# Kernel optimization log

Measured on AMD Instinct MI355X. Metric: run time of the kernel, lower is better.

The kernel has to match this reference:

```python
import jax, jax.numpy as jnp
import numpy as np

B, T, ENC_C = 64, 512, 512   # batch, encoder frames, encoder channels
H = 512                      # hidden_channels
D = 80                       # out_channels (mel dim)
RF = 2                       # reduction_factor
PRE_IN = D * RF              # prenet input (= D*2, see go_frame)
PRE_INNER = 256
CONV_CH = 32                 # location conv channels
K = 31                       # location conv kernel size


def setup_inputs():
    key = jax.random.key(0)
    ks = jax.random.split(key, 16)
    s = 0.02
    f32 = jnp.float32
    p = {}
    p['enc_output'] = jax.random.normal(ks[0], (B, T, ENC_C), f32)
    # acoustic lengths in [T, 2T], multiples of RF -> len//RF in [T//2, T]
    p['data_len'] = (jax.random.randint(ks[1], (B,), T // 2, T + 1, jnp.int32) * RF).astype(jnp.int32)
    # Prenet: two 1x1 convs (== linears) + ReLU
    p['pn_w1'] = jax.random.normal(ks[2], (PRE_INNER, PRE_IN), f32) * s
    p['pn_b1'] = jnp.zeros((PRE_INNER,), f32)
    p['pn_w2'] = jax.random.normal(ks[3], (H, PRE_INNER), f32) * s
    p['pn_b2'] = jnp.zeros((H,), f32)
    # Location-sensitive attention
    p['att_enc_w'] = jax.random.normal(ks[4], (H, ENC_C), f32) * s
    p['att_enc_b'] = jnp.zeros((H,), f32)
    p['att_dec_w'] = jax.random.normal(ks[5], (H, H), f32) * s
    p['att_conv_w'] = jax.random.normal(ks[6], (CONV_CH, 1, K), f32) * s
    p['att_loc_w'] = jax.random.normal(ks[7], (H, CONV_CH), f32) * s
    p['att_v_w'] = jax.random.normal(ks[8], (H,), f32) * s
    p['att_v_b'] = jnp.zeros((), f32)
    # 2 GRU cells (torch GRUCell layout: gates [r|z|n])
    p['gru0_wih'] = jax.random.normal(ks[9], (3 * H, ENC_C + H), f32) * s
    p['gru0_whh'] = jax.random.normal(ks[10], (3 * H, H), f32) * s
    p['gru0_bih'] = jnp.zeros((3 * H,), f32)
    p['gru0_bhh'] = jnp.zeros((3 * H,), f32)
    p['gru1_wih'] = jax.random.normal(ks[11], (3 * H, H), f32) * s
    p['gru1_whh'] = jax.random.normal(ks[12], (3 * H, H), f32) * s
    p['gru1_bih'] = jnp.zeros((3 * H,), f32)
    p['gru1_bhh'] = jnp.zeros((3 * H,), f32)
    # out_layer: 1x1 Conv1d(2H -> D*RF) == linear
    p['out_w'] = jax.random.normal(ks[13], (D * RF, 2 * H), f32) * s
    p['out_b'] = jnp.zeros((D * RF,), f32)
    return p


def _gru(x, h, wih, whh, bih, bhh):
    gi = x @ wih.T + bih
    gh = h @ whh.T + bhh
    ir, iz, inn = jnp.split(gi, 3, axis=-1)
    hr, hz, hn = jnp.split(gh, 3, axis=-1)
    r = jax.nn.sigmoid(ir + hr)
    z = jax.nn.sigmoid(iz + hz)
    n = jnp.tanh(inn + r * hn)
    return (1.0 - z) * n + z * h


def _decode(enc_output, data_len, pn_w1, pn_b1, pn_w2, pn_b2,
            att_enc_w, att_enc_b, att_dec_w, att_conv_w, att_loc_w, att_v_w, att_v_b,
            gru0_wih, gru0_whh, gru0_bih, gru0_bhh,
            gru1_wih, gru1_whh, gru1_bih, gru1_bhh, out_w, out_b):
    dt = enc_output.dtype
    len_r = data_len // RF                                   # (B,) encoder-frame lengths
    pad = jnp.arange(T)[None, :] >= len_r[:, None]           # (B,T) True at padding
    valid = (~pad).astype(dt)
    att_prev0 = valid / len_r.astype(dt)[:, None]            # uniform init attention
    # processed memory (computed once, as in attention.reset_state caching)
    pm = jnp.einsum('btc,hc->bth', enc_output, att_enc_w) + att_enc_b

    def step(carry, t):
        h0, h1, prev_out, att_sum = carry
        prev_w = jnp.where(t == 0, att_prev0, att_sum)       # (B,T)
        # location features: 1D conv over previous (cumulative) attention
        f = jax.lax.conv_general_dilated(prev_w[:, None, :], att_conv_w,
                                         (1,), [(K // 2, K // 2)])  # (B,CONV_CH,T)
        loc = jnp.einsum('bct,hc->bth', f, att_loc_w)
        dec = (h0 @ att_dec_w.T)[:, None, :]                 # query from GRU layer 0 state
        erg = jnp.tanh(loc + pm + dec) @ att_v_w + att_v_b   # (B,T)
        erg = jnp.where(pad, jnp.asarray(-1e9, dt), erg)
        att_w = jax.nn.softmax(erg, axis=-1)
        att_c = jnp.einsum('bt,btc->bc', att_w, enc_output)  # context (B,ENC_C)
        # prenet (dropout in eval == identity)
        x = jax.nn.relu(prev_out @ pn_w1.T + pn_b1)
        x = jax.nn.relu(x @ pn_w2.T + pn_b2)
        h0n = _gru(jnp.concatenate([x, att_c], -1), h0, gru0_wih, gru0_whh, gru0_bih, gru0_bhh)
        h1n = _gru(h0n, h1, gru1_wih, gru1_whh, gru1_bih, gru1_bhh)
        out = jnp.concatenate([h1n, att_c], -1) @ out_w.T + out_b   # (B, D*RF)
        return (h0n, h1n, out, att_sum + att_w), (out, att_w)

    zeros = lambda *s: jnp.zeros(s, dt)
    carry0 = (zeros(B, H), zeros(B, H), zeros(B, D * RF), zeros(B, T))
    _, (outs, att_ws) = jax.lax.scan(step, carry0, jnp.arange(T))
    # outs: (T,B,D*RF); each step reshapes to (B,D,RF) and cats on time
    out = outs.transpose(1, 0, 2).reshape(B, T, D, RF).transpose(0, 2, 1, 3).reshape(B, D, T * RF)
    att_w = att_ws.transpose(1, 2, 0)                        # (B, T, T_steps)
    return out, att_w


def reference(enc_output, data_len, pn_w1, pn_b1, pn_w2, pn_b2,
              att_enc_w, att_enc_b, att_dec_w, att_conv_w, att_loc_w, att_v_w, att_v_b,
              gru0_wih, gru0_whh, gru0_bih, gru0_bhh,
              gru1_wih, gru1_whh, gru1_bih, gru1_bhh, out_w, out_b):
    return _decode(enc_output, data_len, pn_w1, pn_b1, pn_w2, pn_b2,
                   att_enc_w, att_enc_b, att_dec_w, att_conv_w, att_loc_w, att_v_w, att_v_b,
                   gru0_wih, gru0_whh, gru0_bih, gru0_bhh,
                   gru1_wih, gru1_whh, gru1_bih, gru1_bhh, out_w, out_b)
```

## Files before the change

### kernel.cpp

```cpp
#include <hip/hip_runtime.h>
#include <hip/hip_bf16.h>

typedef unsigned short u16;


__device__ __forceinline__ float b2f(u16 u) {
  return __uint_as_float(((unsigned)u) << 16);
}
__device__ __forceinline__ u16 f2b(float f) {
  unsigned u = __float_as_uint(f);
  u += 0x7fffu + ((u >> 16) & 1u);
  return (u16)(u >> 16);
}
template<bool F32>
__device__ __forceinline__ float ldw(const void* p, size_t i) {
  return F32 ? ((const float*)p)[i] : b2f(((const u16*)p)[i]);
}
template<bool F32>
__device__ __forceinline__ float4 ldw4(const void* p, size_t i) {
  if (F32) {
    return *(const float4*)((const float*)p + i);
  } else {
    uint2 u = *(const uint2*)((const u16*)p + i);
    float4 r;
    r.x = __uint_as_float(u.x << 16);
    r.y = __uint_as_float(u.x & 0xffff0000u);
    r.z = __uint_as_float(u.y << 16);
    r.w = __uint_as_float(u.y & 0xffff0000u);
    return r;
  }
}
template<bool F32>
__device__ __forceinline__ void stout(void* p, size_t i, float v) {
  if (F32) ((float*)p)[i] = v; else ((u16*)p)[i] = f2b(v);
}
__device__ __forceinline__ float frcp(float x) { return __builtin_amdgcn_rcpf(x); }
__device__ __forceinline__ float tanh_f(float x) {
  float e = __expf(2.f * x);
  return 1.f - 2.f * frcp(e + 1.f);
}
__device__ __forceinline__ float sig_f(float x) { return frcp(1.f + __expf(-x)); }

__device__ __forceinline__ void st_sc(int* p, int v) {
  __hip_atomic_store(p, v, __ATOMIC_RELAXED, __HIP_MEMORY_SCOPE_AGENT);
}
__device__ __forceinline__ int ld_sc(const int* p) {
  return __hip_atomic_load(p, __ATOMIC_RELAXED, __HIP_MEMORY_SCOPE_AGENT);
}
__device__ __forceinline__ void stf_sc(float* p, float v) {
  __hip_atomic_store(p, v, __ATOMIC_RELAXED, __HIP_MEMORY_SCOPE_AGENT);
}
__device__ __forceinline__ float ldf_sc(const float* p) {
  return __hip_atomic_load(p, __ATOMIC_RELAXED, __HIP_MEMORY_SCOPE_AGENT);
}

__device__ __forceinline__ void stage_n(float* lds, const float* src, int n, int tid) {
  int i = 0;
  for (; i + 4096 <= n; i += 4096) {
    float r[8];
#pragma unroll
    for (int j = 0; j < 8; ++j) r[j] = ldf_sc(src + i + tid + j * 512);
#pragma unroll
    for (int j = 0; j < 8; ++j) lds[i + tid + j * 512] = r[j];
  }
  for (; i < n; i += 2048) {
    float r[4];
#pragma unroll
    for (int j = 0; j < 4; ++j) r[j] = ldf_sc(src + i + tid + j * 512);
#pragma unroll
    for (int j = 0; j < 4; ++j) lds[i + tid + j * 512] = r[j];
  }
}

template<bool F32, int NR>
__device__ __forceinline__ void dotN(float* __restrict__ acc, const float* __restrict__ sb,
                                     const void* __restrict__ wb, size_t rb, int wstride,
                                     int nk, int lane, int vz) {
  float4 wa[NR], wn[NR];
#pragma unroll
  for (int i = 0; i < NR; ++i) wa[i] = ldw4<F32>(wb, rb + (size_t)i * wstride + vz);
  for (int kg = 0; kg < nk; kg += 8) {
#pragma unroll
    for (int i = 0; i < NR; ++i) wn[i] = ldw4<F32>(wb, rb + (size_t)i * wstride + kg + 4 + vz);
    float a0 = sb[(kg + 0) * 64 + lane], a1 = sb[(kg + 1) * 64 + lane],
          a2 = sb[(kg + 2) * 64 + lane], a3 = sb[(kg + 3) * 64 + lane];
#pragma unroll
    for (int i = 0; i < NR; ++i)
      acc[i] = fmaf(wa[i].w, a3, fmaf(wa[i].z, a2, fmaf(wa[i].y, a1, fmaf(wa[i].x, a0, acc[i]))));
    int kn = (kg + 8 < nk) ? kg + 8 : kg;
#pragma unroll
    for (int i = 0; i < NR; ++i) wa[i] = ldw4<F32>(wb, rb + (size_t)i * wstride + kn + vz);
    float b0 = sb[(kg + 4) * 64 + lane], b1 = sb[(kg + 5) * 64 + lane],
          b2 = sb[(kg + 6) * 64 + lane], b3 = sb[(kg + 7) * 64 + lane];
#pragma unroll
    for (int i = 0; i < NR; ++i)
      acc[i] = fmaf(wn[i].w, b3, fmaf(wn[i].z, b2, fmaf(wn[i].y, b1, fmaf(wn[i].x, b0, acc[i]))));
  }
}

constexpr size_t OBAR  = 0;
constexpr size_t OFLG  = OBAR  + 128;
constexpr size_t OASUM = OFLG  + 8192;
constexpr size_t ODEC  = OASUM + 32768;
constexpr size_t OH0   = ODEC  + 32768;
constexpr size_t OH1   = OH0   + 32768;
constexpr size_t OPO   = OH1   + 32768;
constexpr size_t OZEND = OPO   + 10240;
constexpr int    ZERO_SPAN_N = (int)OZEND;
constexpr size_t OPRV  = OZEND;
constexpr size_t OERG  = OPRV  + 32768;
constexpr size_t OX1   = OERG  + 32768;
constexpr size_t OX2   = OX1   + 16384;
constexpr size_t OATTC = OX2   + 32768;
constexpr size_t OMM   = OATTC + 32768;
constexpr size_t OGI0  = OMM   + 16384;
constexpr size_t OGH0  = OGI0  + 393216;
constexpr size_t OGH1  = OGH0  + 196608;
constexpr size_t OGI1  = OGH1  + 196608;
constexpr size_t OPM   = OGI1  + 393216;
constexpr size_t OTOT  = OPM   + 8388608;

__device__ __forceinline__ void fastbar(int* flags, int* gen, int target,
                                        int wg, int tid) {
  __syncthreads();
  if (tid == 0) st_sc(flags + wg * 32, target);
  if (wg == 0) {
    if (tid < 64) {
      int i0 = tid * 4;
      for (;;) {
        int ok = (ld_sc(flags + (i0 + 0) * 32) >= target)
               & (ld_sc(flags + (i0 + 1) * 32) >= target)
               & (ld_sc(flags + (i0 + 2) * 32) >= target)
               & (ld_sc(flags + (i0 + 3) * 32) >= target);
        if (__ballot(ok) == 0xFFFFFFFFFFFFFFFFull) break;
      }
      if (tid == 0) st_sc(gen, target);
    }
    __syncthreads();
  } else {
    if (tid == 0) {
      while (ld_sc(gen) < target) {}
    }
    __syncthreads();
  }
}

__global__ void k_zero(float* p, int n) {
  for (int i = blockIdx.x * 256 + threadIdx.x; i < n; i += gridDim.x * 256) p[i] = 0.f;
}
__global__ void k_detect(int* flag, const u16* probe) {
  if (blockIdx.x != 0 || threadIdx.x != 0) return;
  int sane = 0;
  for (int i = 0; i < 256; i += 2) {
    u16 u = probe[i];
    int e = (u >> 7) & 0xFF;
    if (u == 0 || (e >= 97 && e <= 140)) ++sane;
  }
  *flag = (sane < 96) ? 1 : 0;
}
__global__ void k_prevw(float* prevw, const int* dlen) {
  int b = blockIdx.x;
  int len = dlen[b] >> 1;
  float inv = 1.f / (float)len;
  for (int i = threadIdx.x; i < 512; i += 256)
    prevw[b * 512 + i] = (i < len) ? inv : 0.f;
}
template<bool F32>
__global__ void k_cvtT512(const int* flag, float* dst, const void* src) {
  if (*flag != (F32 ? 1 : 0)) return;
  for (int i = blockIdx.x * 256 + threadIdx.x; i < 262144; i += gridDim.x * 256) {
    int c = i >> 9, h = i & 511;
    dst[i] = ldw<F32>(src, (size_t)h * 512 + c);
  }
}
template<bool F32>
__global__ void k_mmat(const int* flag, float* M, const void* locw, const void* convw) {
  if (*flag != (F32 ? 1 : 0)) return;
  int i = blockIdx.x * 256 + threadIdx.x;
  if (i >= 16384) return;
  int h = i >> 5, k = i & 31;
  float acc = 0.f;
  if (k < 31) {
    for (int c = 0; c < 32; ++c)
      acc = fmaf(ldw<F32>(locw, h * 32 + c), ldw<F32>(convw, c * 31 + k), acc);
  }
  M[i] = acc;
}
template<bool F32>
__global__ __launch_bounds__(256) void k_pm(const int* flag, u16* pm, const void* enc,
                                            const float* encwT, const void* encb) {
  if (*flag != (F32 ? 1 : 0)) return;
  __shared__ float encf[16 * 512];
  int row0 = blockIdx.x * 16;
  int tid = threadIdx.x;
  for (int i = tid; i < 16 * 512; i += 256) {
    int r = i >> 9, c = i & 511;
    encf[i] = ldw<F32>(enc, (size_t)(row0 + r) * 512 + c);
  }
  __syncthreads();
  float a0[16], a1[16];
  float bb0 = ldw<F32>(encb, tid), bb1 = ldw<F32>(encb, tid + 256);
#pragma unroll
  for (int r = 0; r < 16; ++r) { a0[r] = bb0; a1[r] = bb1; }
  for (int c = 0; c < 512; ++c) {
    float w0 = encwT[c * 512 + tid];
    float w1 = encwT[c * 512 + 256 + tid];
#pragma unroll
    for (int r = 0; r < 16; ++r) {
      float a = encf[r * 512 + c];
      a0[r] = fmaf(w0, a, a0[r]);
      a1[r] = fmaf(w1, a, a1[r]);
    }
  }
#pragma unroll
  for (int r = 0; r < 16; ++r) {
    pm[(size_t)(row0 + r) * 512 + tid]       = f2b(a0[r]);
    pm[(size_t)(row0 + r) * 512 + 256 + tid] = f2b(a1[r]);
  }
}

struct KP {
  const void* __restrict__ enc;
  const int* __restrict__ dlen;
  const u16* __restrict__ pm;
  const void* __restrict__ wih0; const void* __restrict__ whh0;
  const void* __restrict__ wih1; const void* __restrict__ whh1;
  const void* __restrict__ adec; const void* __restrict__ outw;
  const void* __restrict__ pnw2; const void* __restrict__ pnw1;
  const void* __restrict__ pnb1; const void* __restrict__ pnb2;
  const void* __restrict__ bih0; const void* __restrict__ bhh0;
  const void* __restrict__ bih1; const void* __restrict__ bhh1;
  const void* __restrict__ outb; const void* __restrict__ vw;
  const float* __restrict__ Mg;
  int* __restrict__ bar;
  int* __restrict__ flags;
  float* __restrict__ asum; float* __restrict__ dec;
  float* __restrict__ h0T;  float* __restrict__ h1T;  float* __restrict__ poT;
  float* __restrict__ prevw; float* __restrict__ erg;
  float* __restrict__ x1T;  float* __restrict__ x2T;  float* __restrict__ attcT;
  float* __restrict__ gi0p; float* __restrict__ gh0p;
  float* __restrict__ gh1p; float* __restrict__ gi1p;
  void* __restrict__ out;
};

template<bool F32>
__global__ __launch_bounds__(512, 2) void k_loop(KP p) {
  if (*(const volatile int*)(p.bar + 64) != (F32 ? 1 : 0)) return;
  __shared__ float stg[16384];
  __shared__ u16  M_u[32 * 512];
  __shared__ float dec_s[512];
  __shared__ float v_s[512];
  __shared__ float wq[160];
  __shared__ float sm[512];
  __shared__ float red[16];

  const int wg = blockIdx.x, tid = threadIdx.x;
  const int lane = tid & 63;
  const int wv = __builtin_amdgcn_readfirstlane(tid >> 6);
  const int b_att = wg >> 2, q = wg & 3, t0 = q * 128;
  const int trow = tid >> 6;
  const int hcol = tid & 63;
  float* dec1 = p.gh0p;
  int* genp = p.bar + 32;
  int bt = 0;
  int vz;
  asm volatile("v_mov_b32 %0, 0" : "=v"(vz));

  for (int i = tid; i < 32 * 512; i += 512) {
    int k = i >> 9, h = i & 511;
    M_u[i] = f2b(p.Mg[h * 32 + k]);
  }
  for (int i = tid; i < 512; i += 512) v_s[i] = ldw<F32>(p.vw, i);
  __syncthreads();

  for (int t = 0; t < 512; ++t) {
    if (wg < 32) stage_n(stg, p.poT, 10240, tid);
    if (tid < 158) {
      int g = t0 - 15 + tid;
      wq[tid] = (g >= 0 && g < 512) ? ldf_sc(p.prevw + b_att * 512 + g) : 0.f;
    }
    if (tid < 512)
      dec_s[tid] = ldf_sc(p.dec + b_att * 512 + tid) + ldf_sc(dec1 + b_att * 512 + tid);
    __syncthreads();
    if (wg < 32) {
      int n = wg * 8 + wv;
      float a[1] = {0.f};
      dotN<F32, 1>(a, stg, p.pnw1, (size_t)n * 160, 160, 160, lane, vz);
      stf_sc(p.x1T + n * 64 + lane, fmaxf(a[0] + ldw<F32>(p.pnb1, n), 0.f));
    }
    {
      float wreg[46];
#pragma unroll
      for (int i = 0; i < 46; ++i) wreg[i] = wq[trow * 16 + i];
      float acc[16];
#pragma unroll
      for (int s = 0; s < 16; ++s) acc[s] = 0.f;
      const u16* pmb = p.pm + ((size_t)(b_att * 512 + t0 + trow * 16)) * 512;
      for (int j = 0; j < 8; ++j) {
        int hj = hcol + 64 * j;
        float Mreg[31];
#pragma unroll
        for (int k = 0; k < 31; ++k) Mreg[k] = b2f(M_u[k * 512 + hj]);
        float dj = dec_s[hj], vj = v_s[hj];
#pragma unroll
        for (int s = 0; s < 16; ++s) {
          float u = dj;
#pragma unroll
          for (int k = 0; k < 31; ++k) u = fmaf(Mreg[k], wreg[s + k], u);
          u += b2f(pmb[s * 512 + hj]);
          acc[s] = fmaf(vj, tanh_f(u), acc[s]);
        }
      }
#pragma unroll
      for (int s = 0; s < 16; ++s) {
        float v = acc[s];
#pragma unroll
        for (int off = 32; off; off >>= 1) v += __shfl_xor(v, off, 64);
        if (hcol == 0) sm[trow * 16 + s] = v;
      }
      __syncthreads();
      if (tid < 128) stf_sc(p.erg + b_att * 512 + t0 + tid, sm[tid]);
    }
    fastbar(p.flags, genp, ++bt, wg, tid);

    if (wg < 64) {
      int b = wg;
      int len = p.dlen[b] >> 1;
      float e0 = ldf_sc(p.erg + b * 512 + tid);
      bool v0 = tid < len;
      float mx = v0 ? e0 : -1e30f;
#pragma unroll
      for (int off = 32; off; off >>= 1) mx = fmaxf(mx, __shfl_xor(mx, off, 64));
      if (lane == 0) red[wv] = mx;
      __syncthreads();
      mx = fmaxf(fmaxf(fmaxf(red[0], red[1]), fmaxf(red[2], red[3])),
                 fmaxf(fmaxf(red[4], red[5]), fmaxf(red[6], red[7])));
      float x0 = v0 ? __expf(e0 - mx) : 0.f;
      float s = x0;
#pragma unroll
      for (int off = 32; off; off >>= 1) s += __shfl_xor(s, off, 64);
      if (lane == 0) red[8 + wv] = s;
      __syncthreads();
      s = ((red[8] + red[9]) + (red[10] + red[11])) + ((red[12] + red[13]) + (red[14] + red[15]));
      float w0 = x0 * frcp(s);
      stout<F32>(p.out, 5242880 + (size_t)b * 262144 + (size_t)tid * 512 + t, w0);
      float s0 = p.asum[b * 512 + tid] + w0;
      p.asum[b * 512 + tid] = s0;
      stf_sc(p.prevw + b * 512 + tid, s0);
    } else if (wg < 192) {
      int idx = wg - 64, b = idx >> 1, half = idx & 1;
      int len = p.dlen[b] >> 1;
      float e0 = ldf_sc(p.erg + b * 512 + tid);
      bool v0 = tid < len;
      float mx = v0 ? e0 : -1e30f;
#pragma unroll
      for (int off = 32; off; off >>= 1) mx = fmaxf(mx, __shfl_xor(mx, off, 64));
      if (lane == 0) red[wv] = mx;
      __syncthreads();
      mx = fmaxf(fmaxf(fmaxf(red[0], red[1]), fmaxf(red[2], red[3])),
                 fmaxf(fmaxf(red[4], red[5]), fmaxf(red[6], red[7])));
      float x0 = v0 ? __expf(e0 - mx) : 0.f;
      float s = x0;
#pragma unroll
      for (int off = 32; off; off >>= 1) s += __shfl_xor(s, off, 64);
      if (lane == 0) red[8 + wv] = s;
      __syncthreads();
      s = ((red[8] + red[9]) + (red[10] + red[11])) + ((red[12] + red[13]) + (red[14] + red[15]));
      sm[tid] = x0 * frcp(s);
      __syncthreads();
      int c4 = half * 256 + lane * 4;
      size_t eb = (size_t)b * 262144 + c4;
      float4 ac[8];
#pragma unroll
      for (int i = 0; i < 8; ++i) ac[i] = make_float4(0.f, 0.f, 0.f, 0.f);
      int tb = wv * 64;
      for (int tt = 0; tt < 64; tt += 8) {
#pragma unroll
        for (int i = 0; i < 8; ++i) {
          float4 e = ldw4<F32>(p.enc, eb + (size_t)(tb + tt + i) * 512);
          float w = sm[tb + tt + i];
          ac[i].x = fmaf(w, e.x, ac[i].x);
          ac[i].y = fmaf(w, e.y, ac[i].y);
          ac[i].z = fmaf(w, e.z, ac[i].z);
          ac[i].w = fmaf(w, e.w, ac[i].w);
        }
      }
      float4 ssum;
      ssum.x = ((ac[0].x + ac[1].x) + (ac[2].x + ac[3].x)) + ((ac[4].x + ac[5].x) + (ac[6].x + ac[7].x));
      ssum.y = ((ac[0].y + ac[1].y) + (ac[2].y + ac[3].y)) + ((ac[4].y + ac[5].y) + (ac[6].y + ac[7].y));
      ssum.z = ((ac[0].z + ac[1].z) + (ac[2].z + ac[3].z)) + ((ac[4].z + ac[5].z) + (ac[6].z + ac[7].z));
      ssum.w = ((ac[0].w + ac[1].w) + (ac[2].w + ac[3].w)) + ((ac[4].w + ac[5].w) + (ac[6].w + ac[7].w));
      __syncthreads();
      *(float4*)&stg[wv * 256 + lane * 4] = ssum;
      __syncthreads();
      if (tid < 256) {
        float r = ((stg[tid] + stg[256 + tid]) + (stg[512 + tid] + stg[768 + tid]))
                + ((stg[1024 + tid] + stg[1280 + tid]) + (stg[1536 + tid] + stg[1792 + tid]));
        stf_sc(p.attcT + (half * 256 + tid) * 64 + b, r);
      }
    } else {
      stage_n(stg, p.x1T, 16384, tid);
      __syncthreads();
      int idx = wg - 192;
      int n = idx * 8 + wv;
      float a[1] = {0.f};
      dotN<F32, 1>(a, stg, p.pnw2, (size_t)n * 256, 256, 256, lane, vz);
      stf_sc(p.x2T + n * 64 + lane, fmaxf(a[0] + ldw<F32>(p.pnb2, n), 0.f));
    }
    fastbar(p.flags, genp, ++bt, wg, tid);

    {
      const float* src; const void* wb; float* dst;
      int n0, wstride, wc0;
      if (wg < 128) {
        int kpart = wg & 3, ngrp = wg >> 2;
        src = ((kpart < 2) ? p.x2T : p.attcT) + (kpart & 1) * 16384;
        wb = p.wih0; wstride = 1024;
        wc0 = (kpart >> 1) * 512 + (kpart & 1) * 256;
        n0 = ngrp * 48 + wv * 6;
        dst = p.gi0p + ((size_t)kpart * 1536 + n0) * 64;
      } else if (wg < 192) {
        int idx = wg - 128, kpart = idx & 1, ngrp = idx >> 1;
        src = p.h0T + kpart * 16384;
        wb = p.whh0; wstride = 512; wc0 = kpart * 256;
        n0 = ngrp * 48 + wv * 6;
        dst = p.gh0p + ((size_t)kpart * 1536 + n0) * 64;
      } else {
        int idx = wg - 192, kpart = idx & 1, ngrp = idx >> 1;
        src = p.h1T + kpart * 16384;
        wb = p.whh1; wstride = 512; wc0 = kpart * 256;
        n0 = ngrp * 48 + wv * 6;
        dst = p.gh1p + ((size_t)kpart * 1536 + n0) * 64;
      }
      stage_n(stg, src, 16384, tid);
      __syncthreads();
      float acc[6];
#pragma unroll
      for (int i = 0; i < 6; ++i) acc[i] = 0.f;
      dotN<F32, 6>(acc, stg, wb, (size_t)n0 * wstride + wc0, wstride, 256, lane, vz);
#pragma unroll
      for (int i = 0; i < 6; ++i) stf_sc(dst + (size_t)i * 64 + lane, acc[i]);
    }
    fastbar(p.flags, genp, ++bt, wg, tid);

    if (wg < 64) {
      int e = wg * 512 + tid;
      int h = e >> 6, b = e & 63;
      float ir = ldf_sc(p.gi0p + h * 64 + b) + ldf_sc(p.gi0p + (1536 + h) * 64 + b)
               + ldf_sc(p.gi0p + (3072 + h) * 64 + b) + ldf_sc(p.gi0p + (4608 + h) * 64 + b)
               + ldw<F32>(p.bih0, h);
      float iz = ldf_sc(p.gi0p + (512 + h) * 64 + b) + ldf_sc(p.gi0p + (2048 + h) * 64 + b)
               + ldf_sc(p.gi0p + (3584 + h) * 64 + b) + ldf_sc(p.gi0p + (5120 + h) * 64 + b)
               + ldw<F32>(p.bih0, 512 + h);
      float in = ldf_sc(p.gi0p + (1024 + h) * 64 + b) + ldf_sc(p.gi0p + (2560 + h) * 64 + b)
               + ldf_sc(p.gi0p + (4096 + h) * 64 + b) + ldf_sc(p.gi0p + (5632 + h) * 64 + b)
               + ldw<F32>(p.bih0, 1024 + h);
      float hr = ldf_sc(p.gh0p + h * 64 + b) + ldf_sc(p.gh0p + (1536 + h) * 64 + b)
               + ldw<F32>(p.bhh0, h);
      float hz = ldf_sc(p.gh0p + (512 + h) * 64 + b) + ldf_sc(p.gh0p + (2048 + h) * 64 + b)
               + ldw<F32>(p.bhh0, 512 + h);
      float hn = ldf_sc(p.gh0p + (1024 + h) * 64 + b) + ldf_sc(p.gh0p + (2560 + h) * 64 + b)
               + ldw<F32>(p.bhh0, 1024 + h);
      float r = sig_f(ir + hr), z = sig_f(iz + hz);
      float nn = tanh_f(in + r * hn);
      float ho = ldf_sc(p.h0T + h * 64 + b);
      stf_sc(p.h0T + h * 64 + b, (1.f - z) * nn + z * ho);
    }
    fastbar(p.flags, genp, ++bt, wg, tid);

    if (wg < 128) {
      int kpart = wg & 3, ngrp = wg >> 2;
      stage_n(stg, p.h0T + kpart * 8192, 8192, tid);
      __syncthreads();
      int n0 = ngrp * 48 + wv * 6;
      float acc[6];
#pragma unroll
      for (int i = 0; i < 6; ++i) acc[i] = 0.f;
      dotN<F32, 6>(acc, stg, p.wih1, (size_t)n0 * 512 + kpart * 128, 512, 128, lane, vz);
#pragma unroll
      for (int i = 0; i < 6; ++i)
        stf_sc(p.gi1p + ((size_t)kpart * 1536 + n0 + i) * 64 + lane, acc[i]);
    } else {
      int g = wg - 128;
      int cpart = g >> 6;
      int n = (g & 63) * 8 + wv;
      stage_n(stg, p.h0T + cpart * 16384, 16384, tid);
      __syncthreads();
      float r[1] = {0.f};
      dotN<F32, 1>(r, stg, p.adec, (size_t)n * 512 + cpart * 256, 512, 256, lane, vz);
      float* dst = cpart ? dec1 : p.dec;
      stf_sc(dst + lane * 512 + n, r[0]);
    }
    fastbar(p.flags, genp, ++bt, wg, tid);

    if (wg < 64) {
      int e = wg * 512 + tid;
      int h = e >> 6, b = e & 63;
      float ir = ldf_sc(p.gi1p + h * 64 + b) + ldf_sc(p.gi1p + (1536 + h) * 64 + b)
               + ldf_sc(p.gi1p + (3072 + h) * 64 + b) + ldf_sc(p.gi1p + (4608 + h) * 64 + b)
               + ldw<F32>(p.bih1, h);
      float iz = ldf_sc(p.gi1p + (512 + h) * 64 + b) + ldf_sc(p.gi1p + (2048 + h) * 64 + b)
               + ldf_sc(p.gi1p + (3584 + h) * 64 + b) + ldf_sc(p.gi1p + (5120 + h) * 64 + b)
               + ldw<F32>(p.bih1, 512 + h);
      float in = ldf_sc(p.gi1p + (1024 + h) * 64 + b) + ldf_sc(p.gi1p + (2560 + h) * 64 + b)
               + ldf_sc(p.gi1p + (4096 + h) * 64 + b) + ldf_sc(p.gi1p + (5632 + h) * 64 + b)
               + ldw<F32>(p.bih1, 1024 + h);
      float hr = ldf_sc(p.gh1p + h * 64 + b) + ldf_sc(p.gh1p + (1536 + h) * 64 + b)
               + ldw<F32>(p.bhh1, h);
      float hz = ldf_sc(p.gh1p + (512 + h) * 64 + b) + ldf_sc(p.gh1p + (2048 + h) * 64 + b)
               + ldw<F32>(p.bhh1, 512 + h);
      float hn = ldf_sc(p.gh1p + (1024 + h) * 64 + b) + ldf_sc(p.gh1p + (2560 + h) * 64 + b)
               + ldw<F32>(p.bhh1, 1024 + h);
      float r = sig_f(ir + hr), z = sig_f(iz + hz);
      float nn = tanh_f(in + r * hn);
      float ho = ldf_sc(p.h1T + h * 64 + b);
      stf_sc(p.h1T + h * 64 + b, (1.f - z) * nn + z * ho);
    }
    fastbar(p.flags, genp, ++bt, wg, tid);

    if (wg < 20) {
      int n = wg * 8 + wv;
      float r[1] = {0.f};
      for (int c = 0; c < 4; ++c) {
        const float* src = ((c < 2) ? p.h1T : p.attcT) + (c & 1) * 16384;
        stage_n(stg, src, 16384, tid);
        __syncthreads();
        dotN<F32, 1>(r, stg, p.outw, (size_t)n * 1024 + c * 256, 1024, 256, lane, vz);
        __syncthreads();
      }
      float acc = r[0] + ldw<F32>(p.outb, n);
      stf_sc(p.poT + n * 64 + lane, acc);
      stout<F32>(p.out, (size_t)lane * 81920 + (size_t)(n >> 1) * 1024 + t * 2 + (n & 1), acc);
    }
    fastbar(p.flags, genp, ++bt, wg, tid);
  }
}

extern "C" void kernel_launch(void* const* d_in, const int* in_sizes, int n_in,
                              void* d_out, int out_size, void* d_ws, size_t ws_size,
                              hipStream_t stream) {
  (void)in_sizes; (void)n_in; (void)out_size; (void)ws_size;
  const void* enc   = d_in[0];
  const int*  dlen  = (const int*)d_in[1];
  const void* pnw1  = d_in[2];
  const void* pnb1  = d_in[3];
  const void* pnw2  = d_in[4];
  const void* pnb2  = d_in[5];
  const void* aencw = d_in[6];
  const void* aencb = d_in[7];
  const void* adecw = d_in[8];
  const void* aconv = d_in[9];
  const void* alocw = d_in[10];
  const void* avw   = d_in[11];
  const void* wih0  = d_in[13];
  const void* whh0  = d_in[14];
  const void* bih0  = d_in[15];
  const void* bhh0  = d_in[16];
  const void* wih1  = d_in[17];
  const void* whh1  = d_in[18];
  const void* bih1  = d_in[19];
  const void* bhh1  = d_in[20];
  const void* outw  = d_in[21];
  const void* outb  = d_in[22];

  float* W = (float*)d_ws;
  int* flag = (int*)(W + OBAR) + 64;
  dim3 blk(256);

  k_zero<<<256, blk, 0, stream>>>(W + OBAR, ZERO_SPAN_N);
  k_zero<<<64, blk, 0, stream>>>(W + OGH0, 32768);
  k_detect<<<1, blk, 0, stream>>>(flag, (const u16*)pnw1);
  k_prevw<<<64, blk, 0, stream>>>(W + OPRV, dlen);
  k_mmat<false><<<64, blk, 0, stream>>>(flag, W + OMM, alocw, aconv);
  k_mmat<true ><<<64, blk, 0, stream>>>(flag, W + OMM, alocw, aconv);
  k_cvtT512<false><<<512, blk, 0, stream>>>(flag, W + OGI0, aencw);
  k_cvtT512<true ><<<512, blk, 0, stream>>>(flag, W + OGI0, aencw);
  k_pm<false><<<2048, blk, 0, stream>>>(flag, (u16*)(W + OPM), enc, W + OGI0, aencb);
  k_pm<true ><<<2048, blk, 0, stream>>>(flag, (u16*)(W + OPM), enc, W + OGI0, aencb);

  KP kp;
  kp.enc = enc; kp.dlen = dlen;
  kp.pm = (const u16*)(W + OPM);
  kp.wih0 = wih0; kp.whh0 = whh0;
  kp.wih1 = wih1; kp.whh1 = whh1;
  kp.adec = adecw; kp.outw = outw;
  kp.pnw2 = pnw2; kp.pnw1 = pnw1;
  kp.pnb1 = pnb1; kp.pnb2 = pnb2;
  kp.bih0 = bih0; kp.bhh0 = bhh0;
  kp.bih1 = bih1; kp.bhh1 = bhh1;
  kp.outb = outb; kp.vw = avw;
  kp.Mg = W + OMM;
  kp.bar = (int*)(W + OBAR);
  kp.flags = (int*)(W + OFLG);
  kp.asum = W + OASUM; kp.dec = W + ODEC;
  kp.h0T = W + OH0; kp.h1T = W + OH1; kp.poT = W + OPO;
  kp.prevw = W + OPRV; kp.erg = W + OERG;
  kp.x1T = W + OX1; kp.x2T = W + OX2; kp.attcT = W + OATTC;
  kp.gi0p = W + OGI0; kp.gh0p = W + OGH0;
  kp.gh1p = W + OGH1; kp.gi1p = W + OGI1;
  kp.out = d_out;

  k_loop<false><<<dim3(256), dim3(512), 0, stream>>>(kp);
  k_loop<true ><<<dim3(256), dim3(512), 0, stream>>>(kp);
}
```

Before: 95.07 ms.

## Double workgroup size to 1024 threads and halve per-wave work

Launches the persistent decode kernel with 1024-thread workgroups instead of 512 and redistributes every phase to match. Each wave now handles half as many attention rows and GEMV output rows, and fewer workgroups cover the prenet, GRU elementwise and output stages. Reductions are widened to 16 waves. The aim is more latency hiding per phase, but the tighter launch bounds may limit registers per thread and cause spills in the register-heavy attention loop.

```diff
diff --git a/kernel.cpp b/kernel.cpp
--- a/kernel.cpp
+++ b/kernel.cpp
@@ -56,19 +56,19 @@
 
 __device__ __forceinline__ void stage_n(float* lds, const float* src, int n, int tid) {
   int i = 0;
-  for (; i + 4096 <= n; i += 4096) {
+  for (; i + 8192 <= n; i += 8192) {
     float r[8];
 #pragma unroll
-    for (int j = 0; j < 8; ++j) r[j] = ldf_sc(src + i + tid + j * 512);
-#pragma unroll
-    for (int j = 0; j < 8; ++j) lds[i + tid + j * 512] = r[j];
+    for (int j = 0; j < 8; ++j) r[j] = ldf_sc(src + i + tid + j * 1024);
+#pragma unroll
+    for (int j = 0; j < 8; ++j) lds[i + tid + j * 1024] = r[j];
   }
   for (; i < n; i += 2048) {
-    float r[4];
-#pragma unroll
-    for (int j = 0; j < 4; ++j) r[j] = ldf_sc(src + i + tid + j * 512);
-#pragma unroll
-    for (int j = 0; j < 4; ++j) lds[i + tid + j * 512] = r[j];
+    float r[2];
+#pragma unroll
+    for (int j = 0; j < 2; ++j) r[j] = ldf_sc(src + i + tid + j * 1024);
+#pragma unroll
+    for (int j = 0; j < 2; ++j) lds[i + tid + j * 1024] = r[j];
   }
 }
 
@@ -244,7 +244,7 @@
 };
 
 template<bool F32>
-__global__ __launch_bounds__(512, 2) void k_loop(KP p) {
+__global__ __launch_bounds__(1024, 4) void k_loop(KP p) {
   if (*(const volatile int*)(p.bar + 64) != (F32 ? 1 : 0)) return;
   __shared__ float stg[16384];
   __shared__ u16  M_u[32 * 512];
@@ -252,7 +252,7 @@
   __shared__ float v_s[512];
   __shared__ float wq[160];
   __shared__ float sm[512];
-  __shared__ float red[16];
+  __shared__ float red[32];
 
   const int wg = blockIdx.x, tid = threadIdx.x;
   const int lane = tid & 63;
@@ -266,15 +266,15 @@
   int vz;
   asm volatile("v_mov_b32 %0, 0" : "=v"(vz));
 
-  for (int i = tid; i < 32 * 512; i += 512) {
+  for (int i = tid; i < 32 * 512; i += 1024) {
     int k = i >> 9, h = i & 511;
     M_u[i] = f2b(p.Mg[h * 32 + k]);
   }
-  for (int i = tid; i < 512; i += 512) v_s[i] = ldw<F32>(p.vw, i);
+  if (tid < 512) v_s[tid] = ldw<F32>(p.vw, tid);
   __syncthreads();
 
   for (int t = 0; t < 512; ++t) {
-    if (wg < 32) stage_n(stg, p.poT, 10240, tid);
+    if (wg < 16) stage_n(stg, p.poT, 10240, tid);
     if (tid < 158) {
       int g = t0 - 15 + tid;
       wq[tid] = (g >= 0 && g < 512) ? ldf_sc(p.prevw + b_att * 512 + g) : 0.f;
@@ -282,20 +282,20 @@
     if (tid < 512)
       dec_s[tid] = ldf_sc(p.dec + b_att * 512 + tid) + ldf_sc(dec1 + b_att * 512 + tid);
     __syncthreads();
-    if (wg < 32) {
-      int n = wg * 8 + wv;
+    if (wg < 16) {
+      int n = wg * 16 + wv;
       float a[1] = {0.f};
       dotN<F32, 1>(a, stg, p.pnw1, (size_t)n * 160, 160, 160, lane, vz);
       stf_sc(p.x1T + n * 64 + lane, fmaxf(a[0] + ldw<F32>(p.pnb1, n), 0.f));
     }
     {
-      float wreg[46];
-#pragma unroll
-      for (int i = 0; i < 46; ++i) wreg[i] = wq[trow * 16 + i];
-      float acc[16];
-#pragma unroll
-      for (int s = 0; s < 16; ++s) acc[s] = 0.f;
-      const u16* pmb = p.pm + ((size_t)(b_att * 512 + t0 + trow * 16)) * 512;
+      float wreg[38];
+#pragma unroll
+      for (int i = 0; i < 38; ++i) wreg[i] = wq[trow * 8 + i];
+      float acc[8];
+#pragma unroll
+      for (int s = 0; s < 8; ++s) acc[s] = 0.f;
+      const u16* pmb = p.pm + ((size_t)(b_att * 512 + t0 + trow * 8)) * 512;
       for (int j = 0; j < 8; ++j) {
         int hj = hcol + 64 * j;
         float Mreg[31];
@@ -303,7 +303,7 @@
         for (int k = 0; k < 31; ++k) Mreg[k] = b2f(M_u[k * 512 + hj]);
         float dj = dec_s[hj], vj = v_s[hj];
 #pragma unroll
-        for (int s = 0; s < 16; ++s) {
+        for (int s = 0; s < 8; ++s) {
           float u = dj;
 #pragma unroll
           for (int k = 0; k < 31; ++k) u = fmaf(Mreg[k], wreg[s + k], u);
@@ -312,11 +312,11 @@
         }
       }
 #pragma unroll
-      for (int s = 0; s < 16; ++s) {
+      for (int s = 0; s < 8; ++s) {
         float v = acc[s];
 #pragma unroll
         for (int off = 32; off; off >>= 1) v += __shfl_xor(v, off, 64);
-        if (hcol == 0) sm[trow * 16 + s] = v;
+        if (hcol == 0) sm[trow * 8 + s] = v;
       }
       __syncthreads();
       if (tid < 128) stf_sc(p.erg + b_att * 512 + t0 + tid, sm[tid]);
@@ -326,55 +326,65 @@
     if (wg < 64) {
       int b = wg;
       int len = p.dlen[b] >> 1;
-      float e0 = ldf_sc(p.erg + b * 512 + tid);
-      bool v0 = tid < len;
+      bool act = tid < 512;
+      float e0 = act ? ldf_sc(p.erg + b * 512 + tid) : -1e30f;
+      bool v0 = act && tid < len;
       float mx = v0 ? e0 : -1e30f;
 #pragma unroll
       for (int off = 32; off; off >>= 1) mx = fmaxf(mx, __shfl_xor(mx, off, 64));
       if (lane == 0) red[wv] = mx;
       __syncthreads();
-      mx = fmaxf(fmaxf(fmaxf(red[0], red[1]), fmaxf(red[2], red[3])),
-                 fmaxf(fmaxf(red[4], red[5]), fmaxf(red[6], red[7])));
+      mx = red[0];
+#pragma unroll
+      for (int k2 = 1; k2 < 16; ++k2) mx = fmaxf(mx, red[k2]);
       float x0 = v0 ? __expf(e0 - mx) : 0.f;
       float s = x0;
 #pragma unroll
       for (int off = 32; off; off >>= 1) s += __shfl_xor(s, off, 64);
-      if (lane == 0) red[8 + wv] = s;
-      __syncthreads();
-      s = ((red[8] + red[9]) + (red[10] + red[11])) + ((red[12] + red[13]) + (red[14] + red[15]));
+      if (lane == 0) red[16 + wv] = s;
+      __syncthreads();
+      s = red[16];
+#pragma unroll
+      for (int k2 = 1; k2 < 16; ++k2) s += red[16 + k2];
       float w0 = x0 * frcp(s);
-      stout<F32>(p.out, 5242880 + (size_t)b * 262144 + (size_t)tid * 512 + t, w0);
-      float s0 = p.asum[b * 512 + tid] + w0;
-      p.asum[b * 512 + tid] = s0;
-      stf_sc(p.prevw + b * 512 + tid, s0);
+      if (act) {
+        stout<F32>(p.out, 5242880 + (size_t)b * 262144 + (size_t)tid * 512 + t, w0);
+        float s0 = p.asum[b * 512 + tid] + w0;
+        p.asum[b * 512 + tid] = s0;
+        stf_sc(p.prevw + b * 512 + tid, s0);
+      }
     } else if (wg < 192) {
       int idx = wg - 64, b = idx >> 1, half = idx & 1;
       int len = p.dlen[b] >> 1;
-      float e0 = ldf_sc(p.erg + b * 512 + tid);
-      bool v0 = tid < len;
+      bool act = tid < 512;
+      float e0 = act ? ldf_sc(p.erg + b * 512 + tid) : -1e30f;
+      bool v0 = act && tid < len;
       float mx = v0 ? e0 : -1e30f;
 #pragma unroll
       for (int off = 32; off; off >>= 1) mx = fmaxf(mx, __shfl_xor(mx, off, 64));
       if (lane == 0) red[wv] = mx;
       __syncthreads();
-      mx = fmaxf(fmaxf(fmaxf(red[0], red[1]), fmaxf(red[2], red[3])),
-                 fmaxf(fmaxf(red[4], red[5]), fmaxf(red[6], red[7])));
+      mx = red[0];
+#pragma unroll
+      for (int k2 = 1; k2 < 16; ++k2) mx = fmaxf(mx, red[k2]);
       float x0 = v0 ? __expf(e0 - mx) : 0.f;
       float s = x0;
 #pragma unroll
       for (int off = 32; off; off >>= 1) s += __shfl_xor(s, off, 64);
-      if (lane == 0) red[8 + wv] = s;
-      __syncthreads();
-      s = ((red[8] + red[9]) + (red[10] + red[11])) + ((red[12] + red[13]) + (red[14] + red[15]));
-      sm[tid] = x0 * frcp(s);
+      if (lane == 0) red[16 + wv] = s;
+      __syncthreads();
+      s = red[16];
+#pragma unroll
+      for (int k2 = 1; k2 < 16; ++k2) s += red[16 + k2];
+      if (act) sm[tid] = x0 * frcp(s);
       __syncthreads();
       int c4 = half * 256 + lane * 4;
       size_t eb = (size_t)b * 262144 + c4;
       float4 ac[8];
 #pragma unroll
       for (int i = 0; i < 8; ++i) ac[i] = make_float4(0.f, 0.f, 0.f, 0.f);
-      int tb = wv * 64;
-      for (int tt = 0; tt < 64; tt += 8) {
+      int tb = wv * 32;
+      for (int tt = 0; tt < 32; tt += 8) {
 #pragma unroll
         for (int i = 0; i < 8; ++i) {
           float4 e = ldw4<F32>(p.enc, eb + (size_t)(tb + tt + i) * 512);
@@ -394,15 +404,16 @@
       *(float4*)&stg[wv * 256 + lane * 4] = ssum;
       __syncthreads();
       if (tid < 256) {
-        float r = ((stg[tid] + stg[256 + tid]) + (stg[512 + tid] + stg[768 + tid]))
-                + ((stg[1024 + tid] + stg[1280 + tid]) + (stg[1536 + tid] + stg[1792 + tid]));
+        float r = 0.f;
+#pragma unroll
+        for (int k2 = 0; k2 < 16; ++k2) r += stg[k2 * 256 + tid];
         stf_sc(p.attcT + (half * 256 + tid) * 64 + b, r);
       }
-    } else {
+    } else if (wg < 224) {
       stage_n(stg, p.x1T, 16384, tid);
       __syncthreads();
       int idx = wg - 192;
-      int n = idx * 8 + wv;
+      int n = idx * 16 + wv;
       float a[1] = {0.f};
       dotN<F32, 1>(a, stg, p.pnw2, (size_t)n * 256, 256, 256, lane, vz);
       stf_sc(p.x2T + n * 64 + lane, fmaxf(a[0] + ldw<F32>(p.pnb2, n), 0.f));
@@ -417,34 +428,34 @@
         src = ((kpart < 2) ? p.x2T : p.attcT) + (kpart & 1) * 16384;
         wb = p.wih0; wstride = 1024;
         wc0 = (kpart >> 1) * 512 + (kpart & 1) * 256;
-        n0 = ngrp * 48 + wv * 6;
+        n0 = ngrp * 48 + wv * 3;
         dst = p.gi0p + ((size_t)kpart * 1536 + n0) * 64;
       } else if (wg < 192) {
         int idx = wg - 128, kpart = idx & 1, ngrp = idx >> 1;
         src = p.h0T + kpart * 16384;
         wb = p.whh0; wstride = 512; wc0 = kpart * 256;
-        n0 = ngrp * 48 + wv * 6;
+        n0 = ngrp * 48 + wv * 3;
         dst = p.gh0p + ((size_t)kpart * 1536 + n0) * 64;
       } else {
         int idx = wg - 192, kpart = idx & 1, ngrp = idx >> 1;
         src = p.h1T + kpart * 16384;
         wb = p.whh1; wstride = 512; wc0 = kpart * 256;
-        n0 = ngrp * 48 + wv * 6;
+        n0 = ngrp * 48 + wv * 3;
         dst = p.gh1p + ((size_t)kpart * 1536 + n0) * 64;
       }
       stage_n(stg, src, 16384, tid);
       __syncthreads();
-      float acc[6];
-#pragma unroll
-      for (int i = 0; i < 6; ++i) acc[i] = 0.f;
-      dotN<F32, 6>(acc, stg, wb, (size_t)n0 * wstride + wc0, wstride, 256, lane, vz);
-#pragma unroll
-      for (int i = 0; i < 6; ++i) stf_sc(dst + (size_t)i * 64 + lane, acc[i]);
+      float acc[3];
+#pragma unroll
+      for (int i = 0; i < 3; ++i) acc[i] = 0.f;
+      dotN<F32, 3>(acc, stg, wb, (size_t)n0 * wstride + wc0, wstride, 256, lane, vz);
+#pragma unroll
+      for (int i = 0; i < 3; ++i) stf_sc(dst + (size_t)i * 64 + lane, acc[i]);
     }
     fastbar(p.flags, genp, ++bt, wg, tid);
 
-    if (wg < 64) {
-      int e = wg * 512 + tid;
+    if (wg < 32) {
+      int e = wg * 1024 + tid;
       int h = e >> 6, b = e & 63;
       float ir = ldf_sc(p.gi0p + h * 64 + b) + ldf_sc(p.gi0p + (1536 + h) * 64 + b)
                + ldf_sc(p.gi0p + (3072 + h) * 64 + b) + ldf_sc(p.gi0p + (4608 + h) * 64 + b)
@@ -472,18 +483,18 @@
       int kpart = wg & 3, ngrp = wg >> 2;
       stage_n(stg, p.h0T + kpart * 8192, 8192, tid);
       __syncthreads();
-      int n0 = ngrp * 48 + wv * 6;
-      float acc[6];
-#pragma unroll
-      for (int i = 0; i < 6; ++i) acc[i] = 0.f;
-      dotN<F32, 6>(acc, stg, p.wih1, (size_t)n0 * 512 + kpart * 128, 512, 128, lane, vz);
-#pragma unroll
-      for (int i = 0; i < 6; ++i)
+      int n0 = ngrp * 48 + wv * 3;
+      float acc[3];
+#pragma unroll
+      for (int i = 0; i < 3; ++i) acc[i] = 0.f;
+      dotN<F32, 3>(acc, stg, p.wih1, (size_t)n0 * 512 + kpart * 128, 512, 128, lane, vz);
+#pragma unroll
+      for (int i = 0; i < 3; ++i)
         stf_sc(p.gi1p + ((size_t)kpart * 1536 + n0 + i) * 64 + lane, acc[i]);
-    } else {
+    } else if (wg < 192) {
       int g = wg - 128;
-      int cpart = g >> 6;
-      int n = (g & 63) * 8 + wv;
+      int cpart = g >> 5;
+      int n = (g & 31) * 16 + wv;
       stage_n(stg, p.h0T + cpart * 16384, 16384, tid);
       __syncthreads();
       float r[1] = {0.f};
@@ -493,8 +504,8 @@
     }
     fastbar(p.flags, genp, ++bt, wg, tid);
 
-    if (wg < 64) {
-      int e = wg * 512 + tid;
+    if (wg < 32) {
+      int e = wg * 1024 + tid;
       int h = e >> 6, b = e & 63;
       float ir = ldf_sc(p.gi1p + h * 64 + b) + ldf_sc(p.gi1p + (1536 + h) * 64 + b)
                + ldf_sc(p.gi1p + (3072 + h) * 64 + b) + ldf_sc(p.gi1p + (4608 + h) * 64 + b)
@@ -518,8 +529,8 @@
     }
     fastbar(p.flags, genp, ++bt, wg, tid);
 
-    if (wg < 20) {
-      int n = wg * 8 + wv;
+    if (wg < 10) {
+      int n = wg * 16 + wv;
       float r[1] = {0.f};
       for (int c = 0; c < 4; ++c) {
         const float* src = ((c < 2) ? p.h1T : p.attcT) + (c & 1) * 16384;
@@ -600,6 +611,6 @@
   kp.gh1p = W + OGH1; kp.gi1p = W + OGI1;
   kp.out = d_out;
 
-  k_loop<false><<<dim3(256), dim3(512), 0, stream>>>(kp);
-  k_loop<true ><<<dim3(256), dim3(512), 0, stream>>>(kp);
-}
+  k_loop<false><<<dim3(256), dim3(1024), 0, stream>>>(kp);
+  k_loop<true ><<<dim3(256), dim3(1024), 0, stream>>>(kp);
+}
```

Result: slower. 113.5 ms (+19.4%).
